# Optimization experiments

Hardware: AMD Instinct MI355X
Metric: run time of the kernel (lower is better)

The kernel has to match this reference:

```python
import jax, jax.numpy as jnp
import numpy as np

STRIDES = (8, 16, 32, 64, 128)
SIZES = ((40, 40), (20, 20), (10, 10), (5, 5), (3, 3))
NUM_CLASSES = 80
SCORE_THR = 0.025
NMS_PRE = 1000
IOU_THR = 0.5
IMG = 320.0  # img_shape hardcoded to (320, 320); clamp uses max_shape[1]
B = 4


def setup_inputs() -> dict:
    key = jax.random.key(0)
    ks = jax.random.split(key, 15)
    inp = {}
    for i, (h, w) in enumerate(SIZES):
        inp[f"cls{i}"] = jax.random.normal(ks[3 * i], (B, NUM_CLASSES, h, w), dtype=jnp.float32)
        # bbox preds are ltrb distances; scale uniform noise to plausible pixel distances
        inp[f"bbox{i}"] = jax.random.uniform(ks[3 * i + 1], (B, 4, h, w), dtype=jnp.float32) * 64.0
        inp[f"ctr{i}"] = jax.random.normal(ks[3 * i + 2], (B, 1, h, w), dtype=jnp.float32)
    return inp


def _priors(h, w, stride):
    # MlvlPointGenerator: (arange + 0.5) * stride, x fastest-varying
    sx = (jnp.arange(w, dtype=jnp.float32) + 0.5) * stride
    sy = (jnp.arange(h, dtype=jnp.float32) + 0.5) * stride
    return jnp.stack([jnp.tile(sx, h), jnp.repeat(sy, w)], axis=-1)  # [h*w, 2]


def _distance2bbox(points, dist):
    x1 = points[:, 0] - dist[:, 0]
    y1 = points[:, 1] - dist[:, 1]
    x2 = points[:, 0] + dist[:, 2]
    y2 = points[:, 1] + dist[:, 3]
    # torch.clamp_ on the whole tensor: min=0, max=max_shape[1]=320
    return jnp.clip(jnp.stack([x1, y1, x2, y2], axis=-1), 0.0, IMG)


def _pairwise_iou(boxes):
    # torchvision-style IoU on [K,4] boxes
    area = (boxes[:, 2] - boxes[:, 0]) * (boxes[:, 3] - boxes[:, 1])
    lt = jnp.maximum(boxes[:, None, :2], boxes[None, :, :2])
    rb = jnp.minimum(boxes[:, None, 2:], boxes[None, :, 2:])
    wh = jnp.maximum(rb - lt, 0.0)
    inter = wh[..., 0] * wh[..., 1]
    union = area[:, None] + area[None, :] - inter
    safe = jnp.where(union > 0.0, union, 1.0)
    return jnp.where(union > 0.0, inter / safe, 0.0)


def _single(cls_l, bbox_l, ctr_l):
    """Post-process one image. Returns fixed-size (dets [K,5], labels [K], keep [K] bool)."""
    scores_l, labels_l, boxes_l, valid_l = [], [], [], []
    for lvl in range(5):
        h, w = SIZES[lvl]
        pri = _priors(h, w, STRIDES[lvl])
        s = jax.nn.sigmoid(jnp.transpose(cls_l[lvl], (1, 2, 0)).reshape(-1, NUM_CLASSES)).reshape(-1)
        bp = jnp.transpose(bbox_l[lvl], (1, 2, 0)).reshape(-1, 4)
        sf = jax.nn.sigmoid(jnp.transpose(ctr_l[lvl], (1, 2, 0)).reshape(-1))
        # filter_scores_and_topk: mask scores <= thr to -1 so they sort last; fixed-size top_k
        k = min(NMS_PRE, s.shape[0])
        top_s, top_i = jax.lax.top_k(jnp.where(s > SCORE_THR, s, -1.0), k)
        anchor = top_i // NUM_CLASSES
        label = top_i % NUM_CLASSES
        valid = top_s > SCORE_THR
        boxes = _distance2bbox(pri[anchor], bp[anchor])
        # scores multiplied by centerness score factor (FCOS)
        scores_l.append(jnp.where(valid, top_s * sf[anchor], -1.0))
        labels_l.append(label)
        boxes_l.append(boxes)
        valid_l.append(valid)
    scores = jnp.concatenate(scores_l)          # [K]
    labels = jnp.concatenate(labels_l)          # [K]
    boxes = jnp.concatenate(boxes_l, axis=0)    # [K,4]
    valid = jnp.concatenate(valid_l)            # [K]
    # sort by final score descending (NMS processes in score order)
    order = jnp.argsort(-scores)
    scores = scores[order]
    labels = labels[order]
    boxes = boxes[order]
    valid = valid[order]
    # batched_nms: per-class coordinate offset trick
    max_coord = boxes.max()
    off = boxes + (labels.astype(jnp.float32) * (max_coord + 1.0))[:, None]
    iou = _pairwise_iou(off)  # [K,K]
    K = scores.shape[0]
    idx = jnp.arange(K)

    def body(i, keep):
        sup = (iou[i] > IOU_THR) & (idx > i) & keep[i]
        return keep & jnp.logical_not(sup)

    keep = jax.lax.fori_loop(0, K, body, valid)
    dets = jnp.concatenate([boxes, scores[:, None]], axis=-1)  # [K,5]
    return dets, labels, keep


def reference(cls0, cls1, cls2, cls3, cls4, bbox0, bbox1, bbox2, bbox3, bbox4, ctr0, ctr1, ctr2, ctr3, ctr4):
    cls_l = (cls0, cls1, cls2, cls3, cls4)
    bbox_l = (bbox0, bbox1, bbox2, bbox3, bbox4)
    ctr_l = (ctr0, ctr1, ctr2, ctr3, ctr4)
    return jax.vmap(_single)(cls_l, bbox_l, ctr_l)
```

## Files before the change

kernel.cpp:

```cpp
#include <hip/hip_runtime.h>
#include <stdint.h>


#define BN 4
#define NC 80
#define TOT 170720
#define KTOT 4720
#define NWIN 74
#define NJT 19
#define TIE_CAP 4096
#define IMGSZ 320.0f
#define PAIR_CAP 131072
#define LDSP 12288

struct InPtrs {
  const float* cls[5];
  const float* bbox[5];
  const float* ctr[5];
};

__device__ __forceinline__ uint32_t f2s(float f) {
  uint32_t x = __float_as_uint(f);
  return (x & 0x80000000u) ? ~x : (x | 0x80000000u);
}
__device__ __forceinline__ float s2f(uint32_t s) {
  uint32_t x = (s & 0x80000000u) ? (s & 0x7fffffffu) : ~s;
  return __uint_as_float(x);
}
__device__ __forceinline__ float sigmoid32(float v) {
  float e = (float)exp(-(double)v);
  return __fdiv_rn(1.0f, __fadd_rn(1.0f, e));
}
__device__ __forceinline__ void lvl_of(int e, int& l, int& le) {
  if (e < 128000)      { l = 0; le = e; }
  else if (e < 160000) { l = 1; le = e - 128000; }
  else if (e < 168000) { l = 2; le = e - 160000; }
  else if (e < 170000) { l = 3; le = e - 168000; }
  else                 { l = 4; le = e - 170000; }
}
__device__ __forceinline__ int kl_of(int l) {
  constexpr int KL[5] = {1000, 1000, 1000, 1000, 720};
  return KL[l];
}
__device__ __forceinline__ float clip32(float v) {
  return fminf(fmaxf(v, 0.0f), IMGSZ);
}
__device__ __forceinline__ void tile_of(int t, int& l, int& p0) {
  if (t < 25)       { l = 0; p0 = t * 64; }
  else if (t < 32)  { l = 1; p0 = (t - 25) * 64; }
  else if (t < 34)  { l = 2; p0 = (t - 32) * 64; }
  else if (t == 34) { l = 3; p0 = 0; }
  else              { l = 4; p0 = 0; }
}
__device__ __forceinline__ int iou_gt(float bx1, float by1, float bx2, float by2,
                                      float bai, float4 o) {
  float ta_ = __fmul_rn(__fsub_rn(o.z, o.x), __fsub_rn(o.w, o.y));
  float ltx = fmaxf(bx1, o.x), lty = fmaxf(by1, o.y);
  float rbx = fminf(bx2, o.z), rby = fminf(by2, o.w);
  float wd = fmaxf(__fsub_rn(rbx, ltx), 0.0f);
  float hg = fmaxf(__fsub_rn(rby, lty), 0.0f);
  float inter = __fmul_rn(wd, hg);
  float asum = __fadd_rn(bai, ta_);
  float uni  = __fsub_rn(asum, inter);
  float iou  = (uni > 0.0f) ? __fdiv_rn(inter, uni) : 0.0f;
  return (iou > 0.5f) ? 1 : 0;
}

__global__ void k_score(InPtrs in, uint32_t* __restrict__ su, uint32_t* __restrict__ hist0) {
  int b = blockIdx.y;
  int tl, p0; tile_of(blockIdx.x, tl, p0);
  constexpr int HWc[5]  = {1600, 400, 100, 25, 9};
  constexpr int LOFF[5] = {0, 128000, 160000, 168000, 170000};
  int hw = HWc[tl];
  int tw = min(64, hw - p0);
  int tid = threadIdx.x;
  __shared__ uint32_t lu[64 * 81];
  __shared__ uint32_t lh[1024];
  for (int i = tid; i < 1024; i += 256) lh[i] = 0;
  __syncthreads();
  int pf = tid & 63;
  if (pf < tw) {
    const float* cp = in.cls[tl] + (size_t)b * NC * hw + p0 + pf;
    for (int c = tid >> 6; c < NC; c += 4) {
      float v = cp[(size_t)c * hw];
      float s = sigmoid32(v);
      float m = (s > 0.025f) ? s : -1.0f;
      uint32_t u = f2s(m);
      lu[pf * 81 + c] = u;
      atomicAdd(&lh[u >> 22], 1u);
    }
  }
  __syncthreads();
  int bl = b * 5 + tl;
  for (int i = tid; i < 1024; i += 256)
    if (lh[i]) atomicAdd(&hist0[(size_t)bl * 1024 + i], lh[i]);
  int n = tw * NC;
  uint32_t* dst = su + (size_t)b * TOT + LOFF[tl] + p0 * NC;
  for (int idx = tid; idx < n; idx += 256)
    dst[idx] = lu[(idx / 80) * 81 + (idx % 80)];
}

__global__ void k_scan1(const uint32_t* __restrict__ su, const uint32_t* __restrict__ mpfx,
                        uint32_t* __restrict__ hist1) {
  int b = blockIdx.y;
  int tid = threadIdx.x;
  int e0 = blockIdx.x * 256;
  int e = e0 + tid;
  int l0, le0; lvl_of(e0, l0, le0);
  __shared__ uint32_t lh[2][1024];
  for (int i = tid; i < 2048; i += 256) lh[i >> 10][i & 1023] = 0;
  __syncthreads();
  if (e < TOT) {
    int l, le; lvl_of(e, l, le);
    uint32_t C = mpfx[b * 5 + l];
    uint32_t u = su[(size_t)b * TOT + e];
    if ((u >> 22) == (C >> 22)) atomicAdd(&lh[l - l0][(u >> 12) & 1023u], 1u);
  }
  __syncthreads();
  for (int s = 0; s < 2; s++) {
    int l = l0 + s;
    if (l >= 5) break;
    int bl = b * 5 + l;
    for (int i = tid; i < 1024; i += 256)
      if (lh[s][i]) atomicAdd(&hist1[(size_t)bl * 1024 + i], lh[s][i]);
  }
}

__global__ void k_scan2(const uint32_t* __restrict__ su, const uint32_t* __restrict__ mpfx,
                        uint32_t* __restrict__ hist2) {
  int b = blockIdx.y;
  int e = blockIdx.x * blockDim.x + threadIdx.x;
  if (e >= TOT) return;
  int l, le; lvl_of(e, l, le);
  int bl = b * 5 + l;
  uint32_t C = mpfx[bl];
  uint32_t u = su[(size_t)b * TOT + e];
  if ((u >> 12) == (C >> 12))
    atomicAdd(&hist2[(size_t)bl * 4096 + (u & 4095u)], 1u);
}

__global__ void k_findp(const uint32_t* __restrict__ hist, uint32_t* __restrict__ mpfx,
                        uint32_t* __restrict__ mk, int nbins, int shift, int pass) {
  int bl = blockIdx.x;
  uint32_t k = (pass == 0) ? (uint32_t)kl_of(bl % 5) : mk[bl];
  const uint32_t* h = hist + (size_t)bl * nbins;
  __shared__ uint32_t gsum[256];
  int tid = threadIdx.x;
  int per = nbins / 256;
  int base = tid * per;
  uint32_t s = 0;
  for (int i = 0; i < per; i++) s += h[base + i];
  gsum[tid] = s;
  __syncthreads();
  uint32_t above = 0;
  for (int t = tid + 1; t < 256; t++) above += gsum[t];
  if (above < k && above + s >= k) {
    uint32_t cum = above;
    for (int bin = base + per - 1; bin >= base; bin--) {
      uint32_t c = h[bin];
      if (cum < k && cum + c >= k) {
        uint32_t pfx = (pass == 0) ? 0u : mpfx[bl];
        mpfx[bl] = pfx | ((uint32_t)bin << shift);
        mk[bl] = k - cum;
        break;
      }
      cum += c;
    }
  }
}

__global__ void k_compact(const uint32_t* __restrict__ su, const uint32_t* __restrict__ mpfx,
                          uint32_t* __restrict__ selcnt, uint32_t* __restrict__ tiecnt,
                          uint32_t* __restrict__ selu, uint32_t* __restrict__ seli,
                          uint32_t* __restrict__ tiei) {
  int b = blockIdx.y;
  int tid = threadIdx.x;
  int e0 = blockIdx.x * 256;
  int e = e0 + tid;
  int l0, le0; lvl_of(e0, l0, le0);
  __shared__ uint32_t cnt[2], tcnt[2], gbase[2], tgbase[2];
  __shared__ uint32_t su_s[2][256], si_s[2][256];
  __shared__ uint32_t ti_s[2][256];
  if (tid < 2) { cnt[tid] = 0u; tcnt[tid] = 0u; }
  __syncthreads();
  if (e < TOT) {
    int l, le; lvl_of(e, l, le);
    int slot = l - l0;
    int bl = b * 5 + l;
    uint32_t u = su[(size_t)b * TOT + e];
    uint32_t C = mpfx[bl];
    if (u > C) {
      uint32_t p = atomicAdd(&cnt[slot], 1u);
      su_s[slot][p] = u;
      si_s[slot][p] = (uint32_t)le;
    } else if (u == C) {
      uint32_t p = atomicAdd(&tcnt[slot], 1u);
      ti_s[slot][p] = (uint32_t)le;
    }
  }
  __syncthreads();
  if (tid < 2) {
    int bl = b * 5 + l0 + tid;
    if (cnt[tid])  gbase[tid]  = atomicAdd(&selcnt[bl], cnt[tid]);
    if (tcnt[tid]) tgbase[tid] = atomicAdd(&tiecnt[bl], tcnt[tid]);
  }
  __syncthreads();
  for (int s = 0; s < 2; s++) {
    int bl = b * 5 + l0 + s;
    uint32_t n = cnt[s];
    for (uint32_t t = tid; t < n; t += 256) {
      uint32_t pos = gbase[s] + t;
      selu[(size_t)bl * 1024 + pos] = su_s[s][t];
      seli[(size_t)bl * 1024 + pos] = si_s[s][t];
    }
    uint32_t tn = tcnt[s];
    for (uint32_t t = tid; t < tn; t += 256) {
      uint32_t pos = tgbase[s] + t;
      if (pos < TIE_CAP) tiei[(size_t)bl * TIE_CAP + pos] = ti_s[s][t];
    }
  }
}

__global__ void k_ties(const uint32_t* __restrict__ mpfx, const uint32_t* __restrict__ mk,
                       const uint32_t* __restrict__ tiecnt, const uint32_t* __restrict__ tiei,
                       uint32_t* __restrict__ selu, uint32_t* __restrict__ seli) {
  int bl = blockIdx.x;
  int l = bl % 5;
  uint32_t C = mpfx[bl];
  uint32_t T = mk[bl];
  uint32_t G = (uint32_t)kl_of(l) - T;
  uint32_t Tc = tiecnt[bl];
  if (Tc > TIE_CAP) Tc = TIE_CAP;
  __shared__ uint32_t sh[TIE_CAP];
  for (uint32_t t = threadIdx.x; t < Tc; t += blockDim.x) sh[t] = tiei[(size_t)bl * TIE_CAP + t];
  __syncthreads();
  for (uint32_t t = threadIdx.x; t < Tc; t += blockDim.x) {
    uint32_t my = sh[t];
    uint32_t rank = 0;
    for (uint32_t q = 0; q < Tc; q++) rank += (sh[q] < my) ? 1u : 0u;
    if (rank < T) {
      selu[(size_t)bl * 1024 + G + rank] = C;
      seli[(size_t)bl * 1024 + G + rank] = my;
    }
  }
}

__global__ void k_emit(InPtrs in, const uint32_t* __restrict__ selu, const uint32_t* __restrict__ seli,
                       float* __restrict__ ccs, uint32_t* __restrict__ ccl,
                       uint32_t* __restrict__ ccv, float* __restrict__ ccb) {
  int bl = blockIdx.x;
  int chunk = blockIdx.y;
  int b = bl / 5, l = bl % 5;
  int k = kl_of(l);
  __shared__ uint64_t z[1024];
  int tid = threadIdx.x;
  for (int t = tid; t < 1024; t += 256) {
    if (t < k) {
      uint32_t u = selu[(size_t)bl * 1024 + t];
      uint32_t idx = seli[(size_t)bl * 1024 + t];
      z[t] = (((uint64_t)u) << 32) | (uint32_t)(~idx);
    } else z[t] = 0ull;
  }
  __syncthreads();
  int tg = chunk * 256 + tid;
  if (tg >= k) return;
  uint64_t zi = z[tg];
  uint32_t u = (uint32_t)(zi >> 32);
  uint32_t idx = ~(uint32_t)zi;
  int rank = 0;
  const uint4* z4 = (const uint4*)z;
  for (int j4 = 0; j4 < 512; j4++) {
    uint4 q = z4[j4];
    uint64_t za = (((uint64_t)q.y) << 32) | q.x;
    uint64_t zb = (((uint64_t)q.w) << 32) | q.z;
    rank += (za > zi) ? 1 : 0;
    rank += (zb > zi) ? 1 : 0;
  }
  constexpr int Wc[5]  = {40, 20, 10, 5, 3};
  constexpr int HWc[5] = {1600, 400, 100, 25, 9};
  constexpr float Sc[5] = {8.f, 16.f, 32.f, 64.f, 128.f};
  constexpr int COFF[5] = {0, 1000, 2000, 3000, 4000};
  int w = Wc[l], hw = HWc[l];
  float ms = s2f(u);
  int valid = (ms > 0.025f) ? 1 : 0;
  int p = (int)idx / NC, c = (int)idx % NC;
  int x = p % w, y = p / w;
  float sf = sigmoid32(in.ctr[l][(size_t)b * hw + p]);
  float score = valid ? __fmul_rn(ms, sf) : -1.0f;
  float px = __fmul_rn(__fadd_rn((float)x, 0.5f), Sc[l]);
  float py = __fmul_rn(__fadd_rn((float)y, 0.5f), Sc[l]);
  size_t bb = (size_t)b * 4 * hw;
  float d0 = in.bbox[l][bb + 0 * hw + p];
  float d1 = in.bbox[l][bb + 1 * hw + p];
  float d2 = in.bbox[l][bb + 2 * hw + p];
  float d3 = in.bbox[l][bb + 3 * hw + p];
  float x1 = clip32(__fsub_rn(px, d0)), y1 = clip32(__fsub_rn(py, d1));
  float x2 = clip32(__fadd_rn(px, d2)), y2 = clip32(__fadd_rn(py, d3));
  int o = b * KTOT + COFF[l] + rank;
  ccs[o] = score;
  ccl[o] = (uint32_t)c;
  ccv[o] = (uint32_t)valid;
  ccb[(size_t)o * 4 + 0] = x1; ccb[(size_t)o * 4 + 1] = y1;
  ccb[(size_t)o * 4 + 2] = x2; ccb[(size_t)o * 4 + 3] = y2;
}

__global__ void k_rank(const float* __restrict__ ccs, uint32_t* __restrict__ rankp) {
  int b = blockIdx.z;
  int jt = blockIdx.y;
  int ib = blockIdx.x;
  int tid = threadIdx.x;
  __shared__ uint32_t jk[256];
  int j0 = jt * 256;
  int jn = min(256, KTOT - j0);
  jk[tid] = (tid < jn) ? f2s(ccs[(size_t)b * KTOT + j0 + tid]) : 0u;
  __syncthreads();
  int e = ib * 256 + tid;
  if (e >= KTOT) return;
  uint32_t ke = f2s(ccs[(size_t)b * KTOT + e]);
  int rank = 0;
  const uint4* k4 = (const uint4*)jk;
#pragma unroll 8
  for (int q = 0; q < 64; q++) {
    uint4 kk = k4[q];
    int j = j0 + q * 4;
    rank += ((kk.x > ke) || (kk.x == ke && (j + 0) < e)) ? 1 : 0;
    rank += ((kk.y > ke) || (kk.y == ke && (j + 1) < e)) ? 1 : 0;
    rank += ((kk.z > ke) || (kk.z == ke && (j + 2) < e)) ? 1 : 0;
    rank += ((kk.w > ke) || (kk.w == ke && (j + 3) < e)) ? 1 : 0;
  }
  rankp[((size_t)b * NJT + jt) * KTOT + e] = (uint32_t)rank;
}

__global__ void k_scatter(const float* __restrict__ ccs, const uint32_t* __restrict__ ccl,
                          const uint32_t* __restrict__ ccv, const float* __restrict__ ccb,
                          const uint32_t* __restrict__ rankp,
                          float* __restrict__ ss, uint32_t* __restrict__ sl,
                          uint32_t* __restrict__ sv, float* __restrict__ sb,
                          uint32_t* __restrict__ maxcb) {
  int b = blockIdx.y;
  __shared__ float red[4];
  int tid = threadIdx.x;
  int e = blockIdx.x * 256 + tid;
  float mx = 0.0f;
  if (e < KTOT) {
    uint32_t rank = 0;
    for (int jt = 0; jt < NJT; jt++)
      rank += rankp[((size_t)b * NJT + jt) * KTOT + e];
    int sidx = b * KTOT + e;
    int d = b * KTOT + (int)rank;
    ss[d] = ccs[sidx];
    sl[d] = ccl[sidx];
    sv[d] = ccv[sidx];
    float b0 = ccb[(size_t)sidx * 4 + 0], b1 = ccb[(size_t)sidx * 4 + 1];
    float b2 = ccb[(size_t)sidx * 4 + 2], b3 = ccb[(size_t)sidx * 4 + 3];
    sb[(size_t)d * 4 + 0] = b0; sb[(size_t)d * 4 + 1] = b1;
    sb[(size_t)d * 4 + 2] = b2; sb[(size_t)d * 4 + 3] = b3;
    mx = fmaxf(fmaxf(b0, b1), fmaxf(b2, b3));
  }
  for (int o = 32; o; o >>= 1) mx = fmaxf(mx, __shfl_xor(mx, o));
  if ((tid & 63) == 0) red[tid >> 6] = mx;
  __syncthreads();
  if (tid == 0)
    atomicMax(&maxcb[b], __float_as_uint(fmaxf(fmaxf(red[0], red[1]), fmaxf(red[2], red[3]))));
}

__global__ void k_offbits(const float* __restrict__ sb, const uint32_t* __restrict__ sl,
                          const uint32_t* __restrict__ maxcb, const uint32_t* __restrict__ sv,
                          float* __restrict__ ob, unsigned long long* __restrict__ vbits,
                          uint32_t* __restrict__ paircnt) {
  int b = blockIdx.y;
  int tid = threadIdx.x;
  if (blockIdx.x == 0 && b == 0 && tid < BN) paircnt[tid] = 0u;
  int e = blockIdx.x * 256 + tid;
  int pred = 0;
  if (e < KTOT) {
    int r = b * KTOT + e;
    float scale = __fadd_rn(__uint_as_float(maxcb[b]), 1.0f);
    float offv = __fmul_rn((float)sl[r], scale);
    float x1 = __fadd_rn(sb[(size_t)r * 4 + 0], offv);
    float y1 = __fadd_rn(sb[(size_t)r * 4 + 1], offv);
    float x2 = __fadd_rn(sb[(size_t)r * 4 + 2], offv);
    float y2 = __fadd_rn(sb[(size_t)r * 4 + 3], offv);
    ob[(size_t)r * 4 + 0] = x1; ob[(size_t)r * 4 + 1] = y1;
    ob[(size_t)r * 4 + 2] = x2; ob[(size_t)r * 4 + 3] = y2;
    pred = (sv[r] != 0u);
  }
  unsigned long long m = __ballot(pred);
  int w = blockIdx.x * 4 + (tid >> 6);
  if ((tid & 63) == 0 && w < NWIN) vbits[b * NWIN + w] = m;
}

__global__ void k_pairs(const uint32_t* __restrict__ sl, const float* __restrict__ ob,
                        uint32_t* __restrict__ pairs, uint32_t* __restrict__ paircnt) {
  int b = blockIdx.y;
  int c = blockIdx.x;
  int tid = threadIdx.x;
  int lane = tid & 63, wv = tid >> 6;
  __shared__ uint32_t lst[KTOT];
  __shared__ uint32_t woff[4];
  __shared__ float4 tb[256];
  __shared__ uint32_t jidx[256];
  __shared__ uint32_t pcnt[256];
  __shared__ uint32_t sbase;
  uint32_t base = 0;
  for (int chunk = 0; chunk < KTOT; chunk += 256) {
    int e = chunk + tid;
    int pred = (e < KTOT) && (sl[(size_t)b * KTOT + e] == (uint32_t)c);
    unsigned long long bal = __ballot(pred);
    if (lane == 0) woff[wv] = (uint32_t)__popcll(bal);
    __syncthreads();
    uint32_t myoff = base;
    for (int v = 0; v < wv; v++) myoff += woff[v];
    uint32_t tot = woff[0] + woff[1] + woff[2] + woff[3];
    if (pred) lst[myoff + (uint32_t)__popcll(bal & ((1ull << lane) - 1ull))] = (uint32_t)e;
    base += tot;
    __syncthreads();
  }
  int m = (int)base;
  if (m < 2) return;
  const float4* ob4 = (const float4*)ob + (size_t)b * KTOT;
  uint32_t mycnt = 0;
  for (int jt = 0; jt < m; jt += 256) {
    int jn = min(256, m - jt);
    __syncthreads();
    if (tid < jn) { uint32_t gj = lst[jt + tid]; jidx[tid] = gj; tb[tid] = ob4[gj]; }
    __syncthreads();
    for (int i = tid; i < m; i += 256) {
      uint32_t gi = lst[i];
      float4 v = ob4[gi];
      float bai = __fmul_rn(__fsub_rn(v.z, v.x), __fsub_rn(v.w, v.y));
      for (int jj = 0; jj < jn; jj++)
        if (jidx[jj] > gi && iou_gt(v.x, v.y, v.z, v.w, bai, tb[jj])) mycnt++;
    }
  }
  __syncthreads();
  pcnt[tid] = mycnt;
  __syncthreads();
  uint32_t myoff = 0, total = 0;
  for (int t = 0; t < 256; t++) { uint32_t v = pcnt[t]; if (t < tid) myoff += v; total += v; }
  if (total == 0) return;
  if (tid == 0) sbase = atomicAdd(&paircnt[b], total);
  __syncthreads();
  uint32_t gb = sbase;
  uint32_t* gp = pairs + (size_t)b * PAIR_CAP;
  uint32_t k = 0;
  for (int jt = 0; jt < m; jt += 256) {
    int jn = min(256, m - jt);
    __syncthreads();
    if (tid < jn) { uint32_t gj = lst[jt + tid]; jidx[tid] = gj; tb[tid] = ob4[gj]; }
    __syncthreads();
    for (int i = tid; i < m; i += 256) {
      uint32_t gi = lst[i];
      float4 v = ob4[gi];
      float bai = __fmul_rn(__fsub_rn(v.z, v.x), __fsub_rn(v.w, v.y));
      for (int jj = 0; jj < jn; jj++) {
        uint32_t gj = jidx[jj];
        if (gj > gi && iou_gt(v.x, v.y, v.z, v.w, bai, tb[jj])) {
          uint32_t pos = gb + myoff + k; k++;
          if (pos < PAIR_CAP) gp[pos] = (gi << 13) | gj;
        }
      }
    }
  }
}

__global__ void k_nms(const float* __restrict__ ob,
                      const unsigned long long* __restrict__ vbits,
                      unsigned long long* __restrict__ keepw,
                      const uint32_t* __restrict__ pairs,
                      const uint32_t* __restrict__ paircnt) {
  int b = blockIdx.x;
  int tid = threadIdx.x;
  int lane = tid & 63;
  __shared__ unsigned long long tdl[NWIN * 64];
  __shared__ unsigned long long svl[NWIN];
  __shared__ unsigned long long sup[NWIN];
  __shared__ unsigned long long kwsh;
  __shared__ uint32_t plp[LDSP];
  __shared__ uint32_t wstart[NWIN + 1];
  __shared__ uint32_t wtmp[NWIN];
  for (int i = tid; i < NWIN * 64; i += 256) tdl[i] = 0ull;
  if (tid < NWIN) { svl[tid] = vbits[b * NWIN + tid]; sup[tid] = 0ull; wtmp[tid] = 0u; }
  uint32_t npairs = paircnt[b];
  bool useP = (npairs <= (uint32_t)PAIR_CAP);
  bool useL = (npairs <= (uint32_t)LDSP);
  const uint32_t* gpl = pairs + (size_t)b * PAIR_CAP;
  __syncthreads();
  unsigned int* sup32 = (unsigned int*)sup;
  unsigned int* tdl32 = (unsigned int*)tdl;
  if (useP) {
    for (uint32_t t = tid; t < npairs; t += 256) {
      uint32_t p = gpl[t];
      int i = (int)(p >> 13), j = (int)(p & 8191u);
      if ((i >> 6) == (j >> 6)) {
        int r = ((i >> 6) * 64 + (i & 63)) * 2 + ((j & 63) >> 5);
        atomicOr(&tdl32[r], 1u << (j & 31));
      } else {
        atomicAdd(&wtmp[i >> 6], 1u);
      }
    }
    __syncthreads();
    if (tid == 0) {
      uint32_t acc = 0;
      for (int w = 0; w < NWIN; w++) { wstart[w] = acc; acc += wtmp[w]; }
      wstart[NWIN] = acc;
    }
    __syncthreads();
    if (tid < NWIN) wtmp[tid] = 0u;
    __syncthreads();
    if (useL) {
      for (uint32_t t = tid; t < npairs; t += 256) {
        uint32_t p = gpl[t];
        int i = (int)(p >> 13), j = (int)(p & 8191u);
        if ((i >> 6) == (j >> 6)) continue;
        uint32_t w = (uint32_t)(i >> 6);
        uint32_t pos = wstart[w] + atomicAdd(&wtmp[w], 1u);
        plp[pos] = p;
      }
    }
    __syncthreads();
    if (tid < 64) {
      for (int w = 0; w < NWIN; w++) {
        unsigned long long row = tdl[w * 64 + lane];
        unsigned long long m = __ballot(row != 0ull);
        unsigned long long sa = sup[w];
        unsigned long long sval = svl[w];
        unsigned int rlo = (unsigned int)row, rhi = (unsigned int)(row >> 32);
        while (m) {
          int i = __ffsll((long long)m) - 1;
          m &= m - 1;
          if (((sval >> i) & 1ull) && !((sa >> i) & 1ull)) {
            unsigned int lo = (unsigned int)__builtin_amdgcn_readlane((int)rlo, i);
            unsigned int hi = (unsigned int)__builtin_amdgcn_readlane((int)rhi, i);
            sa |= (((unsigned long long)hi) << 32) | (unsigned long long)lo;
          }
        }
        unsigned long long kw = sval & ~sa;
        if (lane == 0) keepw[b * NWIN + w] = kw;
        if (useL) {
          for (uint32_t t = wstart[w] + lane; t < wstart[w + 1]; t += 64) {
            uint32_t p = plp[t];
            int i = (int)(p >> 13);
            if (!((kw >> (i & 63)) & 1ull)) continue;
            int j = (int)(p & 8191u);
            atomicOr(&sup32[j >> 5], 1u << (j & 31));
          }
        } else {
          for (uint32_t t = lane; t < npairs; t += 64) {
            uint32_t p = gpl[t];
            int i = (int)(p >> 13);
            if ((i >> 6) != w) continue;
            int j = (int)(p & 8191u);
            if ((j >> 6) == w) continue;
            if (!((kw >> (i & 63)) & 1ull)) continue;
            atomicOr(&sup32[j >> 5], 1u << (j & 31));
          }
        }
        __threadfence_block();
      }
    }
  } else {
    int wv = tid >> 6;
    const float4* ob4 = (const float4*)ob + (size_t)b * KTOT;
    for (int w = 0; w < NWIN; w++) {
      if (wv == 0) {
        int i = w * 64 + lane;
        unsigned long long row = 0ull;
        if (i < KTOT) {
          float4 v = ob4[i];
          float bai = __fmul_rn(__fsub_rn(v.z, v.x), __fsub_rn(v.w, v.y));
          for (int jj = 0; jj < 64; jj++) {
            int j = w * 64 + jj;
            if (j > i && j < KTOT)
              row |= ((unsigned long long)iou_gt(v.x, v.y, v.z, v.w, bai, ob4[j])) << jj;
          }
        }
        unsigned long long m = __ballot(row != 0ull);
        unsigned long long sa = sup[w];
        unsigned long long sval = svl[w];
        unsigned int rlo = (unsigned int)row, rhi = (unsigned int)(row >> 32);
        while (m) {
          int i2 = __ffsll((long long)m) - 1;
          m &= m - 1;
          if (((sval >> i2) & 1ull) && !((sa >> i2) & 1ull)) {
            unsigned int lo = (unsigned int)__builtin_amdgcn_readlane((int)rlo, i2);
            unsigned int hi = (unsigned int)__builtin_amdgcn_readlane((int)rhi, i2);
            sa |= (((unsigned long long)hi) << 32) | (unsigned long long)lo;
          }
        }
        unsigned long long kw = sval & ~sa;
        if (lane == 0) { keepw[b * NWIN + w] = kw; kwsh = kw; }
      }
      __syncthreads();
      unsigned long long kw = kwsh;
      for (int ii = 0; ii < 64; ii++) {
        if (!((kw >> ii) & 1ull)) continue;
        int i = w * 64 + ii;
        if (i >= KTOT) break;
        float4 v = ob4[i];
        float bai = __fmul_rn(__fsub_rn(v.z, v.x), __fsub_rn(v.w, v.y));
        for (int j = (w + 1) * 64 + tid; j < KTOT; j += 256)
          if (iou_gt(v.x, v.y, v.z, v.w, bai, ob4[j]))
            atomicOr(&sup32[j >> 5], 1u << (j & 31));
      }
      __syncthreads();
    }
  }
}

__global__ void k_out(const float* __restrict__ ss, const uint32_t* __restrict__ sl,
                      const float* __restrict__ sb, const unsigned long long* __restrict__ keepw,
                      float* __restrict__ out) {
  int r = blockIdx.x * blockDim.x + threadIdx.x;
  if (r >= BN * KTOT) return;
  int b = r / KTOT;
  int e = r - b * KTOT;
  unsigned int kp = (unsigned int)((keepw[b * NWIN + (e >> 6)] >> (e & 63)) & 1ull);
  out[(size_t)r * 5 + 0] = sb[(size_t)r * 4 + 0];
  out[(size_t)r * 5 + 1] = sb[(size_t)r * 4 + 1];
  out[(size_t)r * 5 + 2] = sb[(size_t)r * 4 + 2];
  out[(size_t)r * 5 + 3] = sb[(size_t)r * 4 + 3];
  out[(size_t)r * 5 + 4] = ss[r];
  out[(size_t)BN * KTOT * 5 + r] = (float)sl[r];
  out[(size_t)BN * KTOT * 6 + r] = kp ? 1.0f : 0.0f;
}

extern "C" void kernel_launch(void* const* d_in, const int* in_sizes, int n_in,
                              void* d_out, int out_size, void* d_ws, size_t ws_size,
                              hipStream_t stream) {
  InPtrs ip;
  for (int l = 0; l < 5; l++) {
    ip.cls[l]  = (const float*)d_in[3 * l + 0];
    ip.bbox[l] = (const float*)d_in[3 * l + 1];
    ip.ctr[l]  = (const float*)d_in[3 * l + 2];
  }

  size_t off = 0;
  auto alloc = [&](size_t n) {
    char* p = (char*)d_ws + off;
    off = (off + n + 255) & ~(size_t)255;
    return p;
  };
  const size_t SU_BYTES   = (size_t)BN * TOT * 4;
  const size_t HIST_BYTES = (20ull * 1024 + 20ull * 1024 + 20ull * 4096) * 4;
  const size_t EXTRA      = 256;
  char* r0p = (char*)alloc(((SU_BYTES + 255) & ~(size_t)255) + HIST_BYTES + EXTRA);
  uint32_t* su    = (uint32_t*)r0p;
  uint32_t* hist0 = (uint32_t*)(r0p + ((SU_BYTES + 255) & ~(size_t)255));
  uint32_t* hist1 = hist0 + 20ull * 1024;
  uint32_t* hist2 = hist1 + 20ull * 1024;
  uint32_t* selcnt = hist2 + 20ull * 4096;
  uint32_t* tiecnt = selcnt + 20;
  uint32_t* maxcb  = tiecnt + 20;

  uint32_t* mpfx   = (uint32_t*)alloc(20 * 4);
  uint32_t* mk     = (uint32_t*)alloc(20 * 4);
  uint32_t* selu   = (uint32_t*)alloc(20ull * 1024 * 4);
  uint32_t* seli   = (uint32_t*)alloc(20ull * 1024 * 4);
  uint32_t* tiei   = (uint32_t*)alloc(20ull * TIE_CAP * 4);
  float*    ccs    = (float*)   alloc((size_t)BN * KTOT * 4);
  uint32_t* ccl    = (uint32_t*)alloc((size_t)BN * KTOT * 4);
  uint32_t* ccv    = (uint32_t*)alloc((size_t)BN * KTOT * 4);
  float*    ccb    = (float*)   alloc((size_t)BN * KTOT * 16);
  float*    ss     = (float*)   alloc((size_t)BN * KTOT * 4);
  uint32_t* sl     = (uint32_t*)alloc((size_t)BN * KTOT * 4);
  uint32_t* sv     = (uint32_t*)alloc((size_t)BN * KTOT * 4);
  float*    sb     = (float*)   alloc((size_t)BN * KTOT * 16);
  float*    ob     = (float*)   alloc((size_t)BN * KTOT * 16);
  uint32_t* rankp  = (uint32_t*)alloc((size_t)BN * NJT * KTOT * 4);
  unsigned long long* vbits = (unsigned long long*)alloc((size_t)BN * NWIN * 8);
  unsigned long long* keepw = (unsigned long long*)alloc((size_t)BN * NWIN * 8);
  uint32_t* pairs   = (uint32_t*)alloc((size_t)BN * PAIR_CAP * 4);
  uint32_t* paircnt = (uint32_t*)alloc(BN * 4);
  (void)ws_size; (void)in_sizes; (void)n_in; (void)out_size;

  dim3 gscan((TOT + 255) / 256, BN);
  hipMemsetAsync(hist0, 0, HIST_BYTES + EXTRA, stream);
  k_score<<<dim3(36, BN), 256, 0, stream>>>(ip, su, hist0);
  k_findp<<<20, 256, 0, stream>>>(hist0, mpfx, mk, 1024, 22, 0);
  k_scan1<<<gscan, 256, 0, stream>>>(su, mpfx, hist1);
  k_findp<<<20, 256, 0, stream>>>(hist1, mpfx, mk, 1024, 12, 1);
  k_scan2<<<gscan, 256, 0, stream>>>(su, mpfx, hist2);
  k_findp<<<20, 256, 0, stream>>>(hist2, mpfx, mk, 4096, 0, 2);
  k_compact<<<gscan, 256, 0, stream>>>(su, mpfx, selcnt, tiecnt, selu, seli, tiei);
  k_ties<<<20, 256, 0, stream>>>(mpfx, mk, tiecnt, tiei, selu, seli);
  k_emit<<<dim3(20, 4), 256, 0, stream>>>(ip, selu, seli, ccs, ccl, ccv, ccb);
  k_rank<<<dim3(19, NJT, BN), 256, 0, stream>>>(ccs, rankp);
  k_scatter<<<dim3(19, BN), 256, 0, stream>>>(ccs, ccl, ccv, ccb, rankp, ss, sl, sv, sb, maxcb);
  k_offbits<<<dim3(19, BN), 256, 0, stream>>>(sb, sl, maxcb, sv, ob, vbits, paircnt);
  k_pairs<<<dim3(NC, BN), 256, 0, stream>>>(sl, ob, pairs, paircnt);
  k_nms<<<BN, 256, 0, stream>>>(ob, vbits, keepw, pairs, paircnt);
  k_out<<<(BN * KTOT + 255) / 256, 256, 0, stream>>>(ss, sl, sb, keepw, (float*)d_out);
}
```

Baseline: 260.0 us.

## Bucket boxes per class in offbits and enumerate NMS pairs in one pass

k_offbits now appends each sorted box index to a per-class list using a global atomic counter. k_pairs therefore loads its class members directly instead of every (class, image) block scanning all 4720 labels with ballots and barriers. k_pairs also records overlapping pairs into an LDS buffer through a shared atomic and copies them out once, replacing the old count pass followed by a second emit pass; it falls back to a recompute pass only when the buffer overflows. The cost is atomic contention, a larger workspace for the class lists, and a nondeterministic ordering of members and pairs.

```diff
diff --git a/kernel.cpp b/kernel.cpp
--- a/kernel.cpp
+++ b/kernel.cpp
@@ -12,6 +12,7 @@
 #define IMGSZ 320.0f
 #define PAIR_CAP 131072
 #define LDSP 12288
+#define SPC_CAP 4096
 
 struct InPtrs {
   const float* cls[5];
@@ -367,7 +368,8 @@
 __global__ void k_offbits(const float* __restrict__ sb, const uint32_t* __restrict__ sl,
                           const uint32_t* __restrict__ maxcb, const uint32_t* __restrict__ sv,
                           float* __restrict__ ob, unsigned long long* __restrict__ vbits,
-                          uint32_t* __restrict__ paircnt) {
+                          uint32_t* __restrict__ paircnt,
+                          uint32_t* __restrict__ clist, uint32_t* __restrict__ ccount) {
   int b = blockIdx.y;
   int tid = threadIdx.x;
   if (blockIdx.x == 0 && b == 0 && tid < BN) paircnt[tid] = 0u;
@@ -376,7 +378,8 @@
   if (e < KTOT) {
     int r = b * KTOT + e;
     float scale = __fadd_rn(__uint_as_float(maxcb[b]), 1.0f);
-    float offv = __fmul_rn((float)sl[r], scale);
+    uint32_t c = sl[r];
+    float offv = __fmul_rn((float)c, scale);
     float x1 = __fadd_rn(sb[(size_t)r * 4 + 0], offv);
     float y1 = __fadd_rn(sb[(size_t)r * 4 + 1], offv);
     float x2 = __fadd_rn(sb[(size_t)r * 4 + 2], offv);
@@ -384,66 +387,31 @@
     ob[(size_t)r * 4 + 0] = x1; ob[(size_t)r * 4 + 1] = y1;
     ob[(size_t)r * 4 + 2] = x2; ob[(size_t)r * 4 + 3] = y2;
     pred = (sv[r] != 0u);
+    uint32_t pos = atomicAdd(&ccount[b * NC + c], 1u);
+    clist[((size_t)b * NC + c) * KTOT + pos] = (uint32_t)e;
   }
   unsigned long long m = __ballot(pred);
   int w = blockIdx.x * 4 + (tid >> 6);
   if ((tid & 63) == 0 && w < NWIN) vbits[b * NWIN + w] = m;
 }
 
-__global__ void k_pairs(const uint32_t* __restrict__ sl, const float* __restrict__ ob,
+__global__ void k_pairs(const uint32_t* __restrict__ clist, const uint32_t* __restrict__ ccount,
+                        const float* __restrict__ ob,
                         uint32_t* __restrict__ pairs, uint32_t* __restrict__ paircnt) {
   int b = blockIdx.y;
   int c = blockIdx.x;
-  int tid = threadIdx.x;
-  int lane = tid & 63, wv = tid >> 6;
+  int m = (int)ccount[b * NC + c];
+  if (m < 2) return;
+  int tid = threadIdx.x;
+  const uint32_t* cl = clist + ((size_t)b * NC + c) * KTOT;
+  const float4* ob4 = (const float4*)ob + (size_t)b * KTOT;
   __shared__ uint32_t lst[KTOT];
-  __shared__ uint32_t woff[4];
+  __shared__ uint32_t spc[SPC_CAP];
   __shared__ float4 tb[256];
   __shared__ uint32_t jidx[256];
-  __shared__ uint32_t pcnt[256];
-  __shared__ uint32_t sbase;
-  uint32_t base = 0;
-  for (int chunk = 0; chunk < KTOT; chunk += 256) {
-    int e = chunk + tid;
-    int pred = (e < KTOT) && (sl[(size_t)b * KTOT + e] == (uint32_t)c);
-    unsigned long long bal = __ballot(pred);
-    if (lane == 0) woff[wv] = (uint32_t)__popcll(bal);
-    __syncthreads();
-    uint32_t myoff = base;
-    for (int v = 0; v < wv; v++) myoff += woff[v];
-    uint32_t tot = woff[0] + woff[1] + woff[2] + woff[3];
-    if (pred) lst[myoff + (uint32_t)__popcll(bal & ((1ull << lane) - 1ull))] = (uint32_t)e;
-    base += tot;
-    __syncthreads();
-  }
-  int m = (int)base;
-  if (m < 2) return;
-  const float4* ob4 = (const float4*)ob + (size_t)b * KTOT;
-  uint32_t mycnt = 0;
-  for (int jt = 0; jt < m; jt += 256) {
-    int jn = min(256, m - jt);
-    __syncthreads();
-    if (tid < jn) { uint32_t gj = lst[jt + tid]; jidx[tid] = gj; tb[tid] = ob4[gj]; }
-    __syncthreads();
-    for (int i = tid; i < m; i += 256) {
-      uint32_t gi = lst[i];
-      float4 v = ob4[gi];
-      float bai = __fmul_rn(__fsub_rn(v.z, v.x), __fsub_rn(v.w, v.y));
-      for (int jj = 0; jj < jn; jj++)
-        if (jidx[jj] > gi && iou_gt(v.x, v.y, v.z, v.w, bai, tb[jj])) mycnt++;
-    }
-  }
-  __syncthreads();
-  pcnt[tid] = mycnt;
-  __syncthreads();
-  uint32_t myoff = 0, total = 0;
-  for (int t = 0; t < 256; t++) { uint32_t v = pcnt[t]; if (t < tid) myoff += v; total += v; }
-  if (total == 0) return;
-  if (tid == 0) sbase = atomicAdd(&paircnt[b], total);
-  __syncthreads();
-  uint32_t gb = sbase;
-  uint32_t* gp = pairs + (size_t)b * PAIR_CAP;
-  uint32_t k = 0;
+  __shared__ uint32_t scnt, sbase;
+  for (int t = tid; t < m; t += 256) lst[t] = cl[t];
+  if (tid == 0) scnt = 0u;
   for (int jt = 0; jt < m; jt += 256) {
     int jn = min(256, m - jt);
     __syncthreads();
@@ -456,8 +424,39 @@
       for (int jj = 0; jj < jn; jj++) {
         uint32_t gj = jidx[jj];
         if (gj > gi && iou_gt(v.x, v.y, v.z, v.w, bai, tb[jj])) {
-          uint32_t pos = gb + myoff + k; k++;
-          if (pos < PAIR_CAP) gp[pos] = (gi << 13) | gj;
+          uint32_t pos = atomicAdd(&scnt, 1u);
+          if (pos < SPC_CAP) spc[pos] = (gi << 13) | gj;
+        }
+      }
+    }
+  }
+  __syncthreads();
+  uint32_t total = scnt;
+  if (total == 0u) return;
+  if (tid == 0) sbase = atomicAdd(&paircnt[b], total);
+  __syncthreads();
+  uint32_t gb = sbase;
+  uint32_t* gp = pairs + (size_t)b * PAIR_CAP;
+  if (total <= (uint32_t)SPC_CAP) {
+    for (uint32_t t = tid; t < total; t += 256)
+      if (gb + t < PAIR_CAP) gp[gb + t] = spc[t];
+  } else {
+    if (tid == 0) scnt = 0u;
+    for (int jt = 0; jt < m; jt += 256) {
+      int jn = min(256, m - jt);
+      __syncthreads();
+      if (tid < jn) { uint32_t gj = lst[jt + tid]; jidx[tid] = gj; tb[tid] = ob4[gj]; }
+      __syncthreads();
+      for (int i = tid; i < m; i += 256) {
+        uint32_t gi = lst[i];
+        float4 v = ob4[gi];
+        float bai = __fmul_rn(__fsub_rn(v.z, v.x), __fsub_rn(v.w, v.y));
+        for (int jj = 0; jj < jn; jj++) {
+          uint32_t gj = jidx[jj];
+          if (gj > gi && iou_gt(v.x, v.y, v.z, v.w, bai, tb[jj])) {
+            uint32_t pos = gb + atomicAdd(&scnt, 1u);
+            if (pos < PAIR_CAP) gp[pos] = (gi << 13) | gj;
+          }
         }
       }
     }
@@ -643,7 +642,7 @@
   };
   const size_t SU_BYTES   = (size_t)BN * TOT * 4;
   const size_t HIST_BYTES = (20ull * 1024 + 20ull * 1024 + 20ull * 4096) * 4;
-  const size_t EXTRA      = 256;
+  const size_t EXTRA      = 2048;
   char* r0p = (char*)alloc(((SU_BYTES + 255) & ~(size_t)255) + HIST_BYTES + EXTRA);
   uint32_t* su    = (uint32_t*)r0p;
   uint32_t* hist0 = (uint32_t*)(r0p + ((SU_BYTES + 255) & ~(size_t)255));
@@ -652,6 +651,7 @@
   uint32_t* selcnt = hist2 + 20ull * 4096;
   uint32_t* tiecnt = selcnt + 20;
   uint32_t* maxcb  = tiecnt + 20;
+  uint32_t* ccount = maxcb + BN;
 
   uint32_t* mpfx   = (uint32_t*)alloc(20 * 4);
   uint32_t* mk     = (uint32_t*)alloc(20 * 4);
@@ -668,6 +668,7 @@
   float*    sb     = (float*)   alloc((size_t)BN * KTOT * 16);
   float*    ob     = (float*)   alloc((size_t)BN * KTOT * 16);
   uint32_t* rankp  = (uint32_t*)alloc((size_t)BN * NJT * KTOT * 4);
+  uint32_t* clist  = (uint32_t*)alloc((size_t)BN * NC * KTOT * 4);
   unsigned long long* vbits = (unsigned long long*)alloc((size_t)BN * NWIN * 8);
   unsigned long long* keepw = (unsigned long long*)alloc((size_t)BN * NWIN * 8);
   uint32_t* pairs   = (uint32_t*)alloc((size_t)BN * PAIR_CAP * 4);
@@ -687,8 +688,8 @@
   k_emit<<<dim3(20, 4), 256, 0, stream>>>(ip, selu, seli, ccs, ccl, ccv, ccb);
   k_rank<<<dim3(19, NJT, BN), 256, 0, stream>>>(ccs, rankp);
   k_scatter<<<dim3(19, BN), 256, 0, stream>>>(ccs, ccl, ccv, ccb, rankp, ss, sl, sv, sb, maxcb);
-  k_offbits<<<dim3(19, BN), 256, 0, stream>>>(sb, sl, maxcb, sv, ob, vbits, paircnt);
-  k_pairs<<<dim3(NC, BN), 256, 0, stream>>>(sl, ob, pairs, paircnt);
+  k_offbits<<<dim3(19, BN), 256, 0, stream>>>(sb, sl, maxcb, sv, ob, vbits, paircnt, clist, ccount);
+  k_pairs<<<dim3(NC, BN), 256, 0, stream>>>(clist, ccount, ob, pairs, paircnt);
   k_nms<<<BN, 256, 0, stream>>>(ob, vbits, keepw, pairs, paircnt);
   k_out<<<(BN * KTOT + 255) / 256, 256, 0, stream>>>(ss, sl, sb, keepw, (float*)d_out);
 }
```

New measurement: 240.9 us. 7.4% less time.
